# Performance work log

Hardware: AMD Instinct MI355X
Metric: run time of the kernel (lower is better)

## Reference

```python
import jax, jax.numpy as jnp
import numpy as np

EPS = 1e-5
GROUPS = 32

def octree_conv(x, neigh, W, b):
    # x: [N, Cin], neigh: [N, 27] (-1 => empty neighbor), W: [27, Cin, Cout]
    N = x.shape[0]
    xp = jnp.concatenate([x, jnp.zeros((1, x.shape[1]), x.dtype)], axis=0)  # zero row for empties
    idx = jnp.where(neigh < 0, N, neigh)
    g = xp[idx]                                # [N, 27, Cin] gathered neighbor features
    return jnp.einsum('nkc,kcd->nd', g, W) + b

def octree_group_norm(x, weight, bias, groups=GROUPS):
    # Normalize each group over all non-empty nodes and the channels in the group.
    N, C = x.shape
    xg = x.reshape(N, groups, C // groups)
    mean = jnp.mean(xg, axis=(0, 2), keepdims=True)
    var = jnp.mean(jnp.square(xg - mean), axis=(0, 2), keepdims=True)
    xn = ((xg - mean) * jax.lax.rsqrt(var + EPS)).reshape(N, C)
    return xn * weight + bias

def setup_inputs() -> dict:
    key = jax.random.key(0)
    ks = jax.random.split(key, 8)
    N, Cin, Cmid, Cout, K = 50000, 128, 128, 32, 27
    data = jax.random.normal(ks[0], (N, Cin), dtype=jnp.float32)
    neigh = jax.random.randint(ks[1], (N, K), 0, N, dtype=jnp.int64)
    W1 = jax.random.normal(ks[2], (K, Cin, Cmid), dtype=jnp.float32) * (1.0 / np.sqrt(K * Cin))
    b1 = jnp.zeros((Cmid,), dtype=jnp.float32)
    gn_w = jnp.ones((Cmid,), dtype=jnp.float32)
    gn_b = jnp.zeros((Cmid,), dtype=jnp.float32)
    W2 = jax.random.normal(ks[3], (K, Cmid, Cout), dtype=jnp.float32) * (1.0 / np.sqrt(K * Cmid))
    b2 = jnp.zeros((Cout,), dtype=jnp.float32)
    return {"data": data, "neigh": neigh, "W1": W1, "b1": b1,
            "gn_w": gn_w, "gn_b": gn_b, "W2": W2, "b2": b2}

def reference(data, neigh, W1, b1, gn_w, gn_b, W2, b2):
    x = octree_conv(data, neigh, W1, b1)          # conv1: in -> mid
    x = octree_group_norm(x, gn_w, gn_b)          # GroupNorm over nodes per group
    x = jax.nn.silu(x)                            # SiLU
    x = octree_conv(x, neigh, W2, b2)             # conv2: mid -> out
    return x
```

## Files before the change

### kernel.cpp

```cpp
#include <hip/hip_runtime.h>
#include <stdint.h>

#define N_NODES 50000
#define CIN 128
#define CMID 128
#define COUT 32
#define KNB 27
#define EPSV 1e-5f

typedef __attribute__((ext_vector_type(4))) float f4v;
typedef __attribute__((ext_vector_type(8))) short s8v;
typedef __attribute__((ext_vector_type(4))) short s4v;

__device__ __forceinline__ unsigned short f2bf(float f) {
  union { float f; uint32_t u; } v; v.f = f;
  return (unsigned short)((v.u + 0x7FFFu + ((v.u >> 16) & 1u)) >> 16);
}

__device__ __forceinline__ f4v mfma16(s8v a, s8v b, f4v c) {
  return __builtin_amdgcn_mfma_f32_16x16x32_bf16(a, b, c, 0, 0, 0);
}

__device__ __forceinline__ void gload_lds16(const void* g, void* lds) {
  __builtin_amdgcn_global_load_lds(
      (const __attribute__((address_space(1))) uint32_t*)(uintptr_t)g,
      (__attribute__((address_space(3))) uint32_t*)(uint32_t)(uintptr_t)lds,
      16, 0, 0);
}

__device__ __forceinline__ bool neigh_is64(const void* neigh) {
  const int* p = (const int*)neigh;
  int ok = 1;
#pragma unroll
  for (int i = 0; i < 16; ++i) {
    int hi = p[2 * i + 1];
    if (hi != 0 && hi != -1) ok = 0;
  }
  return ok != 0;
}

__global__ __launch_bounds__(256) void k_transpose(
    const void* __restrict__ neigh, int* __restrict__ neighT)
{
  __shared__ int tT[KNB][257];
  const int r0 = blockIdx.x * 256;
  const bool is64 = neigh_is64(neigh);
  const int tid = threadIdx.x;
  for (int e = tid; e < 256 * KNB; e += 256) {
    int r = e / KNB, k = e - r * KNB;
    if (r0 + r < N_NODES) {
      long long v = is64 ? ((const long long*)neigh)[(size_t)r0 * KNB + e]
                         : (long long)((const int*)neigh)[(size_t)r0 * KNB + e];
      tT[k][r] = (v < 0) ? N_NODES : (int)v;
    }
  }
  __syncthreads();
  for (int e = tid; e < KNB * 256; e += 256) {
    int k = e >> 8, r = e & 255;
    if (r0 + r < N_NODES) neighT[(size_t)k * N_NODES + r0 + r] = tT[k][r];
  }
}

__global__ __launch_bounds__(256) void k_prep(
    const float* __restrict__ data, const float* __restrict__ W1,
    const float* __restrict__ W2,
    short* __restrict__ xb, short* __restrict__ wt1f, short* __restrict__ wt2f,
    float* __restrict__ gsums)
{
  const int TOT0 = (N_NODES + 1) * (CIN / 4);
  const int TOTW1 = KNB * 4 * 8 * 64;
  const int TOTW2 = KNB * 4 * 2 * 64;
  int gtid = blockIdx.x * 256 + threadIdx.x;
  int stride = gridDim.x * 256;
  for (int i = gtid; i < TOT0 + TOTW1 + TOTW2; i += stride) {
    if (i < TOT0) {
      int row = i >> 5, c4 = i & 31;
      s4v o = {};
      if (row < N_NODES) {
        f4v v = *(const f4v*)(data + (size_t)row * CIN + c4 * 4);
        o[0] = (short)f2bf(v[0]); o[1] = (short)f2bf(v[1]);
        o[2] = (short)f2bf(v[2]); o[3] = (short)f2bf(v[3]);
      }
      *(s4v*)(xb + (size_t)row * CIN + c4 * 4) = o;
    } else if (i < TOT0 + TOTW1) {
      int c = i - TOT0;
      int k = c >> 11, rem = c & 2047;
      int kc = rem >> 9, rem2 = rem & 511;
      int n = rem2 >> 6, l = rem2 & 63;
      int cin0 = kc * 32 + (l >> 4) * 8, cout = n * 16 + (l & 15);
      s8v o;
#pragma unroll
      for (int e = 0; e < 8; ++e)
        o[e] = (short)f2bf(W1[(size_t)k * (CIN * CMID) + (cin0 + e) * CMID + cout]);
      *(s8v*)(wt1f + (size_t)c * 8) = o;
    } else {
      int c = i - TOT0 - TOTW1;
      int k = c >> 9, rem = c & 511;
      int kc = rem >> 7, rem2 = rem & 127;
      int n = rem2 >> 6, l = rem2 & 63;
      int cin0 = kc * 32 + (l >> 4) * 8, cout = n * 16 + (l & 15);
      s8v o;
#pragma unroll
      for (int e = 0; e < 8; ++e)
        o[e] = (short)f2bf(W2[(size_t)k * (CMID * COUT) + (cin0 + e) * COUT + cout]);
      *(s8v*)(wt2f + (size_t)c * 8) = o;
    }
  }
  if (gtid < 64) gsums[gtid] = 0.0f;
}

__global__ __launch_bounds__(256, 3) void k_conv1(
    const short* __restrict__ xb, const int* __restrict__ neighT,
    const short* __restrict__ wt1f, short* __restrict__ x1p)
{
  __shared__ short Bs[2][8192];
  const int tid = threadIdx.x;
  const int l = tid & 63, w = tid >> 6;
  const int bx = blockIdx.x;
  const int kh = (bx >= 391) ? 1 : 0;
  const int rb = kh ? bx - 391 : bx;
  const int rw = rb * 128 + w * 32;
  const int k0 = kh ? 13 : 0, k1 = kh ? 27 : 13;
  const int S = 2 * (k1 - k0);
  const int lr = l & 15, lho = l >> 4;

  int ra = rw + lr;       if (ra >= N_NODES) ra = N_NODES - 1;
  int rb2 = rw + 16 + lr; if (rb2 >= N_NODES) rb2 = N_NODES - 1;

  f4v acc[2][8] = {};
  s8v Ac[2][2], An[2][2];
  int ia, ib, ia2 = 0, ib2 = 0;

  auto stageB = [&](int buf, int s) {
    int k = k0 + (s >> 1), h = s & 1;
    const short* src = wt1f + (size_t)((k * 4 + h * 2) * 8) * 512 + l * 8;
#pragma unroll
    for (int j = 0; j < 4; ++j)
      gload_lds16(src + (w * 4 + j) * 512, &Bs[buf][(w * 4 + j) * 512]);
  };
  auto gatherA = [&](s8v A[2][2], int i0, int i1, int h) {
    const short* p0 = xb + (size_t)i0 * CIN + h * 64 + lho * 8;
    const short* p1 = xb + (size_t)i1 * CIN + h * 64 + lho * 8;
#pragma unroll
    for (int kc = 0; kc < 2; ++kc) {
      A[0][kc] = *(const s8v*)(p0 + kc * 32);
      A[1][kc] = *(const s8v*)(p1 + kc * 32);
    }
  };
  auto compute = [&](int cb, s8v A[2][2]) {
#pragma unroll
    for (int kc = 0; kc < 2; ++kc) {
#pragma unroll
      for (int n = 0; n < 8; ++n) {
        s8v bf = *(const s8v*)&Bs[cb][(kc * 8 + n) * 512 + l * 8];
        acc[0][n] = mfma16(A[0][kc], bf, acc[0][n]);
        acc[1][n] = mfma16(A[1][kc], bf, acc[1][n]);
      }
    }
  };

  ia = neighT[(size_t)k0 * N_NODES + ra];
  ib = neighT[(size_t)k0 * N_NODES + rb2];
  stageB(0, 0);
  gatherA(Ac, ia, ib, 0);
  __syncthreads();

  int cur = 0;
  for (int s = 0; s < S; ++s) {
    const int h = s & 1, k = k0 + (s >> 1);
    if (s + 1 < S) stageB(cur ^ 1, s + 1);
    if (h == 0 && k + 1 < k1) {
      ia2 = neighT[(size_t)(k + 1) * N_NODES + ra];
      ib2 = neighT[(size_t)(k + 1) * N_NODES + rb2];
    }
    if (s + 1 < S) {
      if (h == 0) gatherA(An, ia, ib, 1);
      else        gatherA(An, ia2, ib2, 0);
    }
    compute(cur, Ac);
    __syncthreads();
    if (h == 1) { ia = ia2; ib = ib2; }
#pragma unroll
    for (int kc = 0; kc < 2; ++kc) { Ac[0][kc] = An[0][kc]; Ac[1][kc] = An[1][kc]; }
    cur ^= 1;
  }

  short* xp = x1p + (size_t)kh * N_NODES * CMID;
#pragma unroll
  for (int rg = 0; rg < 2; ++rg) {
#pragma unroll
    for (int j = 0; j < 4; ++j) {
      int grow = rw + rg * 16 + lho * 4 + j;
      if (grow < N_NODES) {
#pragma unroll
        for (int n = 0; n < 8; ++n)
          xp[(size_t)grow * CMID + n * 16 + lr] = (short)f2bf(acc[rg][n][j]);
      }
    }
  }
}

__global__ __launch_bounds__(256) void k_sum(
    const short* __restrict__ x1p, const float* __restrict__ b1,
    float* __restrict__ gsums)
{
  __shared__ float sh[64];
  const int tid = threadIdx.x;
  if (tid < 64) sh[tid] = 0.0f;
  __syncthreads();
  const int g = tid & 31;
  const short* p0 = x1p;
  const short* p1 = x1p + (size_t)N_NODES * CMID;
  f4v bv = *(const f4v*)(b1 + g * 4);
  float s = 0.f, ss = 0.f;
  for (int r = blockIdx.x * 8 + (tid >> 5); r < N_NODES; r += gridDim.x * 8) {
    s4v v0 = *(const s4v*)(p0 + (size_t)r * CMID + g * 4);
    s4v v1 = *(const s4v*)(p1 + (size_t)r * CMID + g * 4);
#pragma unroll
    for (int e = 0; e < 4; ++e) {
      float x = __uint_as_float(((uint32_t)(uint16_t)v0[e]) << 16) +
                __uint_as_float(((uint32_t)(uint16_t)v1[e]) << 16) + bv[e];
      s += x; ss += x * x;
    }
  }
  s += __shfl_xor(s, 32); ss += __shfl_xor(ss, 32);
  if ((tid & 32) == 0) { atomicAdd(&sh[g], s); atomicAdd(&sh[32 + g], ss); }
  __syncthreads();
  if (tid < 64) atomicAdd(&gsums[tid], sh[tid]);
}

__global__ __launch_bounds__(256) void k_gnsilu(
    const short* __restrict__ x1p, const float* __restrict__ b1,
    const float* __restrict__ gsums, const float* __restrict__ gn_w,
    const float* __restrict__ gn_b, short* __restrict__ xnb)
{
  const float invc = 1.0f / (N_NODES * 4.0f);
  const short* p0 = x1p;
  const short* p1 = x1p + (size_t)N_NODES * CMID;
  int gtid = blockIdx.x * 256 + threadIdx.x;
  int stride = gridDim.x * 256;
  const int TOT = (N_NODES + 1) * (CMID / 4);
  for (int i = gtid; i < TOT; i += stride) {
    int row = i >> 5, g = i & 31;
    s4v o = {};
    if (row < N_NODES) {
      float mean = gsums[g] * invc;
      float var = gsums[32 + g] * invc - mean * mean;
      float rs = rsqrtf(var + EPSV);
      s4v v0 = *(const s4v*)(p0 + (size_t)row * CMID + g * 4);
      s4v v1 = *(const s4v*)(p1 + (size_t)row * CMID + g * 4);
      f4v bv = *(const f4v*)(b1 + g * 4);
      f4v wv = *(const f4v*)(gn_w + g * 4);
      f4v gv = *(const f4v*)(gn_b + g * 4);
#pragma unroll
      for (int e = 0; e < 4; ++e) {
        float x = __uint_as_float(((uint32_t)(uint16_t)v0[e]) << 16) +
                  __uint_as_float(((uint32_t)(uint16_t)v1[e]) << 16) + bv[e];
        float xn = (x - mean) * rs * wv[e] + gv[e];
        float y = xn / (1.0f + __expf(-xn));
        o[e] = (short)f2bf(y);
      }
    }
    *(s4v*)(xnb + (size_t)row * CMID + g * 4) = o;
  }
}

__global__ __launch_bounds__(256, 4) void k_conv2(
    const short* __restrict__ xnb, const int* __restrict__ neighT,
    const short* __restrict__ wt2f, float* __restrict__ x2p)
{
  __shared__ short Bs[2][4096];
  const int tid = threadIdx.x;
  const int l = tid & 63, w = tid >> 6;
  const int bx = blockIdx.x;
  const int kh = (bx >= 391) ? 1 : 0;
  const int rb = kh ? bx - 391 : bx;
  const int rw = rb * 128 + w * 32;
  const int k0 = kh ? 13 : 0, k1 = kh ? 27 : 13;
  const int S = k1 - k0;
  const int lr = l & 15, lho = l >> 4;

  int ra = rw + lr;       if (ra >= N_NODES) ra = N_NODES - 1;
  int rb2 = rw + 16 + lr; if (rb2 >= N_NODES) rb2 = N_NODES - 1;

  f4v acc[2][2] = {};
  s8v Ac[2][4], An[2][4];
  int ian = 0, ibn = 0, ia2 = 0, ib2 = 0;

  auto stageB = [&](int buf, int k) {
    const short* src = wt2f + (size_t)(k * 8) * 512 + l * 8;
#pragma unroll
    for (int j = 0; j < 2; ++j)
      gload_lds16(src + (w * 2 + j) * 512, &Bs[buf][(w * 2 + j) * 512]);
  };
  auto gatherA = [&](s8v A[2][4], int i0, int i1) {
    const short* p0 = xnb + (size_t)i0 * CMID + lho * 8;
    const short* p1 = xnb + (size_t)i1 * CMID + lho * 8;
#pragma unroll
    for (int kc = 0; kc < 4; ++kc) {
      A[0][kc] = *(const s8v*)(p0 + kc * 32);
      A[1][kc] = *(const s8v*)(p1 + kc * 32);
    }
  };
  auto compute = [&](int cb, s8v A[2][4]) {
#pragma unroll
    for (int kc = 0; kc < 4; ++kc) {
#pragma unroll
      for (int n = 0; n < 2; ++n) {
        s8v bf = *(const s8v*)&Bs[cb][(kc * 2 + n) * 512 + l * 8];
        acc[0][n] = mfma16(A[0][kc], bf, acc[0][n]);
        acc[1][n] = mfma16(A[1][kc], bf, acc[1][n]);
      }
    }
  };

  int iac = neighT[(size_t)k0 * N_NODES + ra];
  int ibc = neighT[(size_t)k0 * N_NODES + rb2];
  if (S > 1) {
    ian = neighT[(size_t)(k0 + 1) * N_NODES + ra];
    ibn = neighT[(size_t)(k0 + 1) * N_NODES + rb2];
  }
  stageB(0, k0);
  gatherA(Ac, iac, ibc);
  __syncthreads();

  int cur = 0;
  for (int s = 0; s < S; ++s) {
    const int k = k0 + s;
    if (s + 1 < S) stageB(cur ^ 1, k + 1);
    if (s + 2 < S) {
      ia2 = neighT[(size_t)(k + 2) * N_NODES + ra];
      ib2 = neighT[(size_t)(k + 2) * N_NODES + rb2];
    }
    if (s + 1 < S) gatherA(An, ian, ibn);
    compute(cur, Ac);
    __syncthreads();
    ian = ia2; ibn = ib2;
#pragma unroll
    for (int kc = 0; kc < 4; ++kc) { Ac[0][kc] = An[0][kc]; Ac[1][kc] = An[1][kc]; }
    cur ^= 1;
  }

  float* xp = x2p + (size_t)kh * N_NODES * COUT;
#pragma unroll
  for (int rg = 0; rg < 2; ++rg) {
#pragma unroll
    for (int j = 0; j < 4; ++j) {
      int grow = rw + rg * 16 + lho * 4 + j;
      if (grow < N_NODES) {
#pragma unroll
        for (int n = 0; n < 2; ++n)
          xp[(size_t)grow * COUT + n * 16 + lr] = acc[rg][n][j];
      }
    }
  }
}

__global__ __launch_bounds__(256) void k_fin(
    const float* __restrict__ x2p, const float* __restrict__ b2,
    float* __restrict__ out)
{
  int i = blockIdx.x * 256 + threadIdx.x;
  const int TOT = N_NODES * COUT / 4;
  if (i < TOT) {
    int c4 = i & 7;
    f4v a = *(const f4v*)(x2p + (size_t)i * 4);
    f4v b = *(const f4v*)(x2p + (size_t)N_NODES * COUT + (size_t)i * 4);
    f4v bias = *(const f4v*)(b2 + c4 * 4);
    f4v o = a + b + bias;
    *(f4v*)(out + (size_t)i * 4) = o;
  }
}

extern "C" void kernel_launch(void* const* d_in, const int* in_sizes, int n_in,
                              void* d_out, int out_size, void* d_ws, size_t ws_size,
                              hipStream_t stream) {
  const float* data = (const float*)d_in[0];
  const void* neigh = d_in[1];
  const float* W1   = (const float*)d_in[2];
  const float* b1   = (const float*)d_in[3];
  const float* gn_w = (const float*)d_in[4];
  const float* gn_b = (const float*)d_in[5];
  const float* W2   = (const float*)d_in[6];
  const float* b2   = (const float*)d_in[7];

  char* p = (char*)d_ws;
  short* xb   = (short*)p; p += (size_t)(N_NODES + 1) * CIN * 2;
  float* x2p  = (float*)xb;
  short* wt1f = (short*)p; p += (size_t)KNB * CMID * CIN * 2;
  short* wt2f = (short*)p; p += (size_t)KNB * COUT * CMID * 2;
  short* x1p  = (short*)p; p += (size_t)2 * N_NODES * CMID * 2;
  short* xnb  = (short*)p; p += (size_t)(N_NODES + 1) * CMID * 2;
  int*   neighT = (int*)p; p += (size_t)KNB * N_NODES * 4;
  float* gsums = (float*)p;

  k_transpose<<<(N_NODES + 255) / 256, 256, 0, stream>>>(neigh, neighT);
  k_prep<<<2048, 256, 0, stream>>>(data, W1, W2, xb, wt1f, wt2f, gsums);
  k_conv1<<<782, 256, 0, stream>>>(xb, neighT, wt1f, x1p);
  k_sum<<<391, 256, 0, stream>>>(x1p, b1, gsums);
  k_gnsilu<<<2048, 256, 0, stream>>>(x1p, b1, gsums, gn_w, gn_b, xnb);
  k_conv2<<<782, 256, 0, stream>>>(xnb, neighT, wt2f, x2p);
  k_fin<<<(N_NODES * COUT / 4 + 255) / 256, 256, 0, stream>>>(x2p, b2, (float*)d_out);
}
```

Before: 254.9 us.

## Reorder conv2 as project-then-gather and widen conv1 steps to full Cin

Conv2 is now computed by first multiplying each node's features by all 27 per-offset weight slices (a dense GEMM producing a 27*32-wide projected buffer in bf16), then gathering and summing the projected rows per neighbour in two halves. This replaces the gather-then-GEMM that loaded 128-channel rows for every neighbour, reducing gathered bytes per neighbour from 128 to 32 values. The risk is an extra bf16 rounding of the projected values and a large intermediate buffer write. Conv1 also processes a whole neighbour offset per pipeline step with a doubled LDS B tile and lower occupancy target. The final add kernel is folded into the gathers.

After: 285.7 us. 1.12x slower.

```diff
diff --git a/kernel.cpp b/kernel.cpp
--- a/kernel.cpp
+++ b/kernel.cpp
@@ -16,6 +16,9 @@
   union { float f; uint32_t u; } v; v.f = f;
   return (unsigned short)((v.u + 0x7FFFu + ((v.u >> 16) & 1u)) >> 16);
 }
+__device__ __forceinline__ float bf2f(short s) {
+  return __uint_as_float(((uint32_t)(uint16_t)s) << 16);
+}
 
 __device__ __forceinline__ f4v mfma16(s8v a, s8v b, f4v c) {
   return __builtin_amdgcn_mfma_f32_16x16x32_bf16(a, b, c, 0, 0, 0);
@@ -69,7 +72,7 @@
 {
   const int TOT0 = (N_NODES + 1) * (CIN / 4);
   const int TOTW1 = KNB * 4 * 8 * 64;
-  const int TOTW2 = KNB * 4 * 2 * 64;
+  const int TOTW2 = 54 * 4 * 64;
   int gtid = blockIdx.x * 256 + threadIdx.x;
   int stride = gridDim.x * 256;
   for (int i = gtid; i < TOT0 + TOTW1 + TOTW2; i += stride) {
@@ -95,25 +98,25 @@
       *(s8v*)(wt1f + (size_t)c * 8) = o;
     } else {
       int c = i - TOT0 - TOTW1;
-      int k = c >> 9, rem = c & 511;
-      int kc = rem >> 7, rem2 = rem & 127;
-      int n = rem2 >> 6, l = rem2 & 63;
-      int cin0 = kc * 32 + (l >> 4) * 8, cout = n * 16 + (l & 15);
+      int l = c & 63, kc = (c >> 6) & 3, t = c >> 8;
+      int col = t * 16 + (l & 15);
+      int k = col >> 5, j = col & 31;
+      int cin0 = kc * 32 + (l >> 4) * 8;
       s8v o;
 #pragma unroll
       for (int e = 0; e < 8; ++e)
-        o[e] = (short)f2bf(W2[(size_t)k * (CMID * COUT) + (cin0 + e) * COUT + cout]);
+        o[e] = (short)f2bf(W2[(size_t)k * (CMID * COUT) + (cin0 + e) * COUT + j]);
       *(s8v*)(wt2f + (size_t)c * 8) = o;
     }
   }
   if (gtid < 64) gsums[gtid] = 0.0f;
 }
 
-__global__ __launch_bounds__(256, 3) void k_conv1(
+__global__ __launch_bounds__(256, 2) void k_conv1(
     const short* __restrict__ xb, const int* __restrict__ neighT,
     const short* __restrict__ wt1f, short* __restrict__ x1p)
 {
-  __shared__ short Bs[2][8192];
+  __shared__ short Bs[2][16384];
   const int tid = threadIdx.x;
   const int l = tid & 63, w = tid >> 6;
   const int bx = blockIdx.x;
@@ -121,35 +124,36 @@
   const int rb = kh ? bx - 391 : bx;
   const int rw = rb * 128 + w * 32;
   const int k0 = kh ? 13 : 0, k1 = kh ? 27 : 13;
-  const int S = 2 * (k1 - k0);
+  const int S = k1 - k0;
   const int lr = l & 15, lho = l >> 4;
 
   int ra = rw + lr;       if (ra >= N_NODES) ra = N_NODES - 1;
   int rb2 = rw + 16 + lr; if (rb2 >= N_NODES) rb2 = N_NODES - 1;
 
   f4v acc[2][8] = {};
-  s8v Ac[2][2], An[2][2];
-  int ia, ib, ia2 = 0, ib2 = 0;
-
-  auto stageB = [&](int buf, int s) {
-    int k = k0 + (s >> 1), h = s & 1;
-    const short* src = wt1f + (size_t)((k * 4 + h * 2) * 8) * 512 + l * 8;
-#pragma unroll
-    for (int j = 0; j < 4; ++j)
-      gload_lds16(src + (w * 4 + j) * 512, &Bs[buf][(w * 4 + j) * 512]);
+  s8v Ac[2][4], An[2][4];
+  int ian = 0, ibn = 0, ia2 = 0, ib2 = 0;
+
+  auto stageB = [&](int buf, int k) {
+#pragma unroll
+    for (int j = 0; j < 8; ++j) {
+      int q = w * 8 + j;
+      const short* src = wt1f + ((size_t)(k * 32 + q) << 9) + l * 8;
+      gload_lds16(src, &Bs[buf][q * 512]);
+    }
   };
-  auto gatherA = [&](s8v A[2][2], int i0, int i1, int h) {
-    const short* p0 = xb + (size_t)i0 * CIN + h * 64 + lho * 8;
-    const short* p1 = xb + (size_t)i1 * CIN + h * 64 + lho * 8;
-#pragma unroll
-    for (int kc = 0; kc < 2; ++kc) {
+  auto gatherA = [&](s8v A[2][4], int i0, int i1) {
+    const short* p0 = xb + (size_t)i0 * CIN + lho * 8;
+    const short* p1 = xb + (size_t)i1 * CIN + lho * 8;
+#pragma unroll
+    for (int kc = 0; kc < 4; ++kc) {
       A[0][kc] = *(const s8v*)(p0 + kc * 32);
       A[1][kc] = *(const s8v*)(p1 + kc * 32);
     }
   };
-  auto compute = [&](int cb, s8v A[2][2]) {
-#pragma unroll
-    for (int kc = 0; kc < 2; ++kc) {
+  auto compute = [&](int cb, s8v A[2][4]) {
+#pragma unroll
+    for (int kc = 0; kc < 4; ++kc) {
 #pragma unroll
       for (int n = 0; n < 8; ++n) {
         s8v bf = *(const s8v*)&Bs[cb][(kc * 8 + n) * 512 + l * 8];
@@ -159,29 +163,32 @@
     }
   };
 
-  ia = neighT[(size_t)k0 * N_NODES + ra];
-  ib = neighT[(size_t)k0 * N_NODES + rb2];
-  stageB(0, 0);
-  gatherA(Ac, ia, ib, 0);
+  {
+    int iac = neighT[(size_t)k0 * N_NODES + ra];
+    int ibc = neighT[(size_t)k0 * N_NODES + rb2];
+    gatherA(Ac, iac, ibc);
+  }
+  if (S > 1) {
+    ian = neighT[(size_t)(k0 + 1) * N_NODES + ra];
+    ibn = neighT[(size_t)(k0 + 1) * N_NODES + rb2];
+  }
+  stageB(0, k0);
   __syncthreads();
 
   int cur = 0;
   for (int s = 0; s < S; ++s) {
-    const int h = s & 1, k = k0 + (s >> 1);
-    if (s + 1 < S) stageB(cur ^ 1, s + 1);
-    if (h == 0 && k + 1 < k1) {
-      ia2 = neighT[(size_t)(k + 1) * N_NODES + ra];
-      ib2 = neighT[(size_t)(k + 1) * N_NODES + rb2];
-    }
-    if (s + 1 < S) {
-      if (h == 0) gatherA(An, ia, ib, 1);
-      else        gatherA(An, ia2, ib2, 0);
-    }
+    const int k = k0 + s;
+    if (s + 1 < S) stageB(cur ^ 1, k + 1);
+    if (s + 2 < S) {
+      ia2 = neighT[(size_t)(k + 2) * N_NODES + ra];
+      ib2 = neighT[(size_t)(k + 2) * N_NODES + rb2];
+    }
+    if (s + 1 < S) gatherA(An, ian, ibn);
     compute(cur, Ac);
     __syncthreads();
-    if (h == 1) { ia = ia2; ib = ib2; }
-#pragma unroll
-    for (int kc = 0; kc < 2; ++kc) { Ac[0][kc] = An[0][kc]; Ac[1][kc] = An[1][kc]; }
+    ian = ia2; ibn = ib2;
+#pragma unroll
+    for (int kc = 0; kc < 4; ++kc) { Ac[0][kc] = An[0][kc]; Ac[1][kc] = An[1][kc]; }
     cur ^= 1;
   }
 
@@ -218,8 +225,7 @@
     s4v v1 = *(const s4v*)(p1 + (size_t)r * CMID + g * 4);
 #pragma unroll
     for (int e = 0; e < 4; ++e) {
-      float x = __uint_as_float(((uint32_t)(uint16_t)v0[e]) << 16) +
-                __uint_as_float(((uint32_t)(uint16_t)v1[e]) << 16) + bv[e];
+      float x = bf2f(v0[e]) + bf2f(v1[e]) + bv[e];
       s += x; ss += x * x;
     }
   }
@@ -239,137 +245,107 @@
   const short* p1 = x1p + (size_t)N_NODES * CMID;
   int gtid = blockIdx.x * 256 + threadIdx.x;
   int stride = gridDim.x * 256;
-  const int TOT = (N_NODES + 1) * (CMID / 4);
+  const int TOT = N_NODES * (CMID / 4);
   for (int i = gtid; i < TOT; i += stride) {
     int row = i >> 5, g = i & 31;
-    s4v o = {};
-    if (row < N_NODES) {
-      float mean = gsums[g] * invc;
-      float var = gsums[32 + g] * invc - mean * mean;
-      float rs = rsqrtf(var + EPSV);
-      s4v v0 = *(const s4v*)(p0 + (size_t)row * CMID + g * 4);
-      s4v v1 = *(const s4v*)(p1 + (size_t)row * CMID + g * 4);
-      f4v bv = *(const f4v*)(b1 + g * 4);
-      f4v wv = *(const f4v*)(gn_w + g * 4);
-      f4v gv = *(const f4v*)(gn_b + g * 4);
-#pragma unroll
-      for (int e = 0; e < 4; ++e) {
-        float x = __uint_as_float(((uint32_t)(uint16_t)v0[e]) << 16) +
-                  __uint_as_float(((uint32_t)(uint16_t)v1[e]) << 16) + bv[e];
-        float xn = (x - mean) * rs * wv[e] + gv[e];
-        float y = xn / (1.0f + __expf(-xn));
-        o[e] = (short)f2bf(y);
+    float mean = gsums[g] * invc;
+    float var = gsums[32 + g] * invc - mean * mean;
+    float rs = rsqrtf(var + EPSV);
+    s4v v0 = *(const s4v*)(p0 + (size_t)row * CMID + g * 4);
+    s4v v1 = *(const s4v*)(p1 + (size_t)row * CMID + g * 4);
+    f4v bv = *(const f4v*)(b1 + g * 4);
+    f4v wv = *(const f4v*)(gn_w + g * 4);
+    f4v gv = *(const f4v*)(gn_b + g * 4);
+    s4v o;
+#pragma unroll
+    for (int e = 0; e < 4; ++e) {
+      float x = bf2f(v0[e]) + bf2f(v1[e]) + bv[e];
+      float xn = (x - mean) * rs * wv[e] + gv[e];
+      float y = xn / (1.0f + __expf(-xn));
+      o[e] = (short)f2bf(y);
+    }
+    *(s4v*)(xnb + (size_t)row * CMID + g * 4) = o;
+  }
+}
+
+template<int T0, int NT>
+__global__ __launch_bounds__(256, 1) void k_proj(
+    const short* __restrict__ xnb, const short* __restrict__ wt2f,
+    short* __restrict__ cbuf)
+{
+  __shared__ short Ws[28 * 4 * 512];
+  const int tid = threadIdx.x;
+  const int l = tid & 63, w = tid >> 6;
+  const int rw = blockIdx.x * 128 + w * 32;
+  const int lr = l & 15, lho = l >> 4;
+  const int NC = NT * 16;
+
+  for (int q = w; q < NT * 4; q += 4)
+    gload_lds16(wt2f + ((size_t)(T0 * 4 + q) << 9) + l * 8, &Ws[q * 512]);
+
+  s8v a[2][4];
+#pragma unroll
+  for (int rs = 0; rs < 2; ++rs) {
+    int row = rw + rs * 16 + lr; if (row >= N_NODES) row = N_NODES - 1;
+    const short* p = xnb + (size_t)row * CMID + lho * 8;
+#pragma unroll
+    for (int kc = 0; kc < 4; ++kc) a[rs][kc] = *(const s8v*)(p + kc * 32);
+  }
+  __syncthreads();
+
+  for (int t = 0; t < NT; ++t) {
+    f4v acc[2] = {};
+#pragma unroll
+    for (int kc = 0; kc < 4; ++kc) {
+      s8v bf = *(const s8v*)&Ws[(t * 4 + kc) * 512 + l * 8];
+      acc[0] = mfma16(a[0][kc], bf, acc[0]);
+      acc[1] = mfma16(a[1][kc], bf, acc[1]);
+    }
+#pragma unroll
+    for (int rs = 0; rs < 2; ++rs) {
+#pragma unroll
+      for (int j = 0; j < 4; ++j) {
+        int row = rw + rs * 16 + lho * 4 + j;
+        if (row < N_NODES)
+          cbuf[(size_t)row * NC + t * 16 + lr] = (short)f2bf(acc[rs][j]);
       }
     }
-    *(s4v*)(xnb + (size_t)row * CMID + g * 4) = o;
-  }
-}
-
-__global__ __launch_bounds__(256, 4) void k_conv2(
-    const short* __restrict__ xnb, const int* __restrict__ neighT,
-    const short* __restrict__ wt2f, float* __restrict__ x2p)
-{
-  __shared__ short Bs[2][4096];
-  const int tid = threadIdx.x;
-  const int l = tid & 63, w = tid >> 6;
-  const int bx = blockIdx.x;
-  const int kh = (bx >= 391) ? 1 : 0;
-  const int rb = kh ? bx - 391 : bx;
-  const int rw = rb * 128 + w * 32;
-  const int k0 = kh ? 13 : 0, k1 = kh ? 27 : 13;
-  const int S = k1 - k0;
-  const int lr = l & 15, lho = l >> 4;
-
-  int ra = rw + lr;       if (ra >= N_NODES) ra = N_NODES - 1;
-  int rb2 = rw + 16 + lr; if (rb2 >= N_NODES) rb2 = N_NODES - 1;
-
-  f4v acc[2][2] = {};
-  s8v Ac[2][4], An[2][4];
-  int ian = 0, ibn = 0, ia2 = 0, ib2 = 0;
-
-  auto stageB = [&](int buf, int k) {
-    const short* src = wt2f + (size_t)(k * 8) * 512 + l * 8;
-#pragma unroll
-    for (int j = 0; j < 2; ++j)
-      gload_lds16(src + (w * 2 + j) * 512, &Bs[buf][(w * 2 + j) * 512]);
-  };
-  auto gatherA = [&](s8v A[2][4], int i0, int i1) {
-    const short* p0 = xnb + (size_t)i0 * CMID + lho * 8;
-    const short* p1 = xnb + (size_t)i1 * CMID + lho * 8;
-#pragma unroll
-    for (int kc = 0; kc < 4; ++kc) {
-      A[0][kc] = *(const s8v*)(p0 + kc * 32);
-      A[1][kc] = *(const s8v*)(p1 + kc * 32);
-    }
-  };
-  auto compute = [&](int cb, s8v A[2][4]) {
-#pragma unroll
-    for (int kc = 0; kc < 4; ++kc) {
-#pragma unroll
-      for (int n = 0; n < 2; ++n) {
-        s8v bf = *(const s8v*)&Bs[cb][(kc * 2 + n) * 512 + l * 8];
-        acc[0][n] = mfma16(A[0][kc], bf, acc[0][n]);
-        acc[1][n] = mfma16(A[1][kc], bf, acc[1][n]);
-      }
-    }
-  };
-
-  int iac = neighT[(size_t)k0 * N_NODES + ra];
-  int ibc = neighT[(size_t)k0 * N_NODES + rb2];
-  if (S > 1) {
-    ian = neighT[(size_t)(k0 + 1) * N_NODES + ra];
-    ibn = neighT[(size_t)(k0 + 1) * N_NODES + rb2];
-  }
-  stageB(0, k0);
-  gatherA(Ac, iac, ibc);
-  __syncthreads();
-
-  int cur = 0;
-  for (int s = 0; s < S; ++s) {
-    const int k = k0 + s;
-    if (s + 1 < S) stageB(cur ^ 1, k + 1);
-    if (s + 2 < S) {
-      ia2 = neighT[(size_t)(k + 2) * N_NODES + ra];
-      ib2 = neighT[(size_t)(k + 2) * N_NODES + rb2];
-    }
-    if (s + 1 < S) gatherA(An, ian, ibn);
-    compute(cur, Ac);
-    __syncthreads();
-    ian = ia2; ibn = ib2;
-#pragma unroll
-    for (int kc = 0; kc < 4; ++kc) { Ac[0][kc] = An[0][kc]; Ac[1][kc] = An[1][kc]; }
-    cur ^= 1;
-  }
-
-  float* xp = x2p + (size_t)kh * N_NODES * COUT;
-#pragma unroll
-  for (int rg = 0; rg < 2; ++rg) {
-#pragma unroll
-    for (int j = 0; j < 4; ++j) {
-      int grow = rw + rg * 16 + lho * 4 + j;
-      if (grow < N_NODES) {
-#pragma unroll
-        for (int n = 0; n < 2; ++n)
-          xp[(size_t)grow * COUT + n * 16 + lr] = acc[rg][n][j];
-      }
-    }
-  }
-}
-
-__global__ __launch_bounds__(256) void k_fin(
-    const float* __restrict__ x2p, const float* __restrict__ b2,
-    float* __restrict__ out)
-{
-  int i = blockIdx.x * 256 + threadIdx.x;
-  const int TOT = N_NODES * COUT / 4;
-  if (i < TOT) {
-    int c4 = i & 7;
-    f4v a = *(const f4v*)(x2p + (size_t)i * 4);
-    f4v b = *(const f4v*)(x2p + (size_t)N_NODES * COUT + (size_t)i * 4);
-    f4v bias = *(const f4v*)(b2 + c4 * 4);
-    f4v o = a + b + bias;
-    *(f4v*)(out + (size_t)i * 4) = o;
-  }
+  }
+}
+
+template<int INIT, int KC, int KSTART>
+__global__ __launch_bounds__(256) void k_gather2(
+    const short* __restrict__ cbuf, const void* __restrict__ neigh,
+    const float* __restrict__ b2, float* __restrict__ out)
+{
+  const int tid = threadIdx.x;
+  const int n = blockIdx.x * 32 + (tid >> 3);
+  const int l8 = tid & 7;
+  if (n >= N_NODES) return;
+  const bool is64 = neigh_is64(neigh);
+  const int NC = KC * 32;
+
+  int id[KC]; float msk[KC];
+#pragma unroll
+  for (int k = 0; k < KC; ++k) {
+    long long v = is64 ? ((const long long*)neigh)[(size_t)n * KNB + KSTART + k]
+                       : (long long)((const int*)neigh)[(size_t)n * KNB + KSTART + k];
+    msk[k] = (v >= 0) ? 1.0f : 0.0f;
+    id[k] = (v >= 0) ? (int)v : 0;
+  }
+  f4v acc;
+  if (INIT) acc = *(const f4v*)(b2 + l8 * 4);
+  else      acc = *(const f4v*)(out + (size_t)n * COUT + l8 * 4);
+  s4v cv[KC];
+#pragma unroll
+  for (int k = 0; k < KC; ++k)
+    cv[k] = *(const s4v*)(cbuf + (size_t)id[k] * NC + k * 32 + l8 * 4);
+#pragma unroll
+  for (int k = 0; k < KC; ++k) {
+#pragma unroll
+    for (int e = 0; e < 4; ++e) acc[e] += msk[k] * bf2f(cv[k][e]);
+  }
+  *(f4v*)(out + (size_t)n * COUT + l8 * 4) = acc;
 }
 
 extern "C" void kernel_launch(void* const* d_in, const int* in_sizes, int n_in,
@@ -385,20 +361,24 @@
   const float* b2   = (const float*)d_in[7];
 
   char* p = (char*)d_ws;
+  char* r0 = p;
   short* xb   = (short*)p; p += (size_t)(N_NODES + 1) * CIN * 2;
-  float* x2p  = (float*)xb;
   short* wt1f = (short*)p; p += (size_t)KNB * CMID * CIN * 2;
-  short* wt2f = (short*)p; p += (size_t)KNB * COUT * CMID * 2;
+  int*   neighT = (int*)p; p += (size_t)KNB * N_NODES * 4;
   short* x1p  = (short*)p; p += (size_t)2 * N_NODES * CMID * 2;
-  short* xnb  = (short*)p; p += (size_t)(N_NODES + 1) * CMID * 2;
-  int*   neighT = (int*)p; p += (size_t)KNB * N_NODES * 4;
+  p = r0 + ((size_t)N_NODES * 448 * 2 + 255 & ~(size_t)255);
+  short* cbuf = (short*)r0;
+  short* xnb  = (short*)p; p += (size_t)N_NODES * CMID * 2;
+  short* wt2f = (short*)p; p += (size_t)54 * 4 * 64 * 8 * 2;
   float* gsums = (float*)p;
 
   k_transpose<<<(N_NODES + 255) / 256, 256, 0, stream>>>(neigh, neighT);
   k_prep<<<2048, 256, 0, stream>>>(data, W1, W2, xb, wt1f, wt2f, gsums);
   k_conv1<<<782, 256, 0, stream>>>(xb, neighT, wt1f, x1p);
   k_sum<<<391, 256, 0, stream>>>(x1p, b1, gsums);
-  k_gnsilu<<<2048, 256, 0, stream>>>(x1p, b1, gsums, gn_w, gn_b, xnb);
-  k_conv2<<<782, 256, 0, stream>>>(xnb, neighT, wt2f, x2p);
-  k_fin<<<(N_NODES * COUT / 4 + 255) / 256, 256, 0, stream>>>(x2p, b2, (float*)d_out);
-}
+  k_gnsilu<<<1563, 256, 0, stream>>>(x1p, b1, gsums, gn_w, gn_b, xnb);
+  k_proj<0, 28><<<391, 256, 0, stream>>>(xnb, wt2f, cbuf);
+  k_gather2<1, 14, 0><<<1563, 256, 0, stream>>>(cbuf, neigh, b2, (float*)d_out);
+  k_proj<28, 26><<<391, 256, 0, stream>>>(xnb, wt2f, cbuf);
+  k_gather2<0, 13, 14><<<1563, 256, 0, stream>>>(cbuf, neigh, b2, (float*)d_out);
+}
```
